# Kernel optimization log

Hardware: AMD Instinct MI355X
Metric: run time of the kernel (lower is better)

## Reference

```python
import jax, jax.numpy as jnp
import numpy as np

EPS = 1e-6      # torch F.pairwise_distance default eps (added to the difference)
MARGIN = 1.0

def _cdist_eps(a, b):
    # Exact ||a_i - b_j + eps||_2 via expansion:
    # ||a-b+eps||^2 = ||a||^2 + ||b||^2 - 2 a.b + 2*eps*(sum(a)-sum(b)) + D*eps^2
    D = a.shape[-1]
    sq = (jnp.sum(a * a, axis=1)[:, None]
          + jnp.sum(b * b, axis=1)[None, :]
          - 2.0 * (a @ b.T)
          + 2.0 * EPS * (jnp.sum(a, axis=1)[:, None] - jnp.sum(b, axis=1)[None, :])
          + D * EPS * EPS)
    return jnp.sqrt(jnp.maximum(sq, 0.0))

def setup_inputs() -> dict:
    key = jax.random.key(0)
    k1, k2, k3 = jax.random.split(key, 3)
    B, D = 4096, 1024
    return {
        'anchor_embeddings': jax.random.normal(k1, (B, D), dtype=jnp.float32),
        'positive_embeddings': jax.random.normal(k2, (B, D), dtype=jnp.float32),
        'negative_embeddings': jax.random.normal(k3, (B, D), dtype=jnp.float32),
    }

def reference(anchor_embeddings, positive_embeddings, negative_embeddings):
    a, p, n = anchor_embeddings, positive_embeddings, negative_embeddings
    # per-row anchor-positive and anchor-negative distances
    d_ap = jnp.linalg.norm(a - p + EPS, axis=-1)          # [B]
    d_an_row = jnp.linalg.norm(a - n + EPS, axis=-1)      # [B]

    # hardest negative: for each anchor, max over negatives with dist < d_ap[i], else 0
    dan_mat = _cdist_eps(a, n)                            # [B, B]
    mask_n = dan_mat < d_ap[:, None]
    hard_n = jnp.where(mask_n.any(axis=1),
                       jnp.max(jnp.where(mask_n, dan_mat, -jnp.inf), axis=1),
                       0.0)
    d_an = jnp.mean(hard_n)                               # scalar

    # hardest positive: for each anchor, min over positives with dist > d(a_i, n_i), else 0
    dpp_mat = _cdist_eps(a, p)                            # [B, B]
    mask_p = dpp_mat > d_an_row[:, None]
    hard_p = jnp.where(mask_p.any(axis=1),
                       jnp.min(jnp.where(mask_p, dpp_mat, jnp.inf), axis=1),
                       0.0)
    d_pp = jnp.mean(hard_p)                               # scalar

    loss = jnp.mean(jnp.clip(d_ap - 0.5 * d_pp - 0.5 * d_an + MARGIN, 0.0, None))
    return loss
```

## Files before the change

kernel.cpp:

```cpp
#include <hip/hip_runtime.h>


#define NB 4096
#define DIM 1024
#define EPSF 1e-6f
#define D_EPS2 (1024.0f * 1e-6f * 1e-6f)

#define BM 128
#define BK 32

typedef __bf16  bf16x8 __attribute__((ext_vector_type(8)));
typedef float   f32x4  __attribute__((ext_vector_type(4)));

__device__ __forceinline__ unsigned short f2bf(float x) {
    unsigned u = __float_as_uint(x);
    u += 0x7FFFu + ((u >> 16) & 1u);
    return (unsigned short)(u >> 16);
}

__device__ __forceinline__ void g2l16(const unsigned short* g, unsigned short* l) {
    __builtin_amdgcn_global_load_lds(
        (const __attribute__((address_space(1))) unsigned int*)g,
        (__attribute__((address_space(3))) unsigned int*)l, 16, 0, 0);
}


__global__ __launch_bounds__(256) void row_stats_kernel(
    const float* __restrict__ a, const float* __restrict__ p,
    const float* __restrict__ n,
    unsigned short* __restrict__ abf, unsigned short* __restrict__ pbf,
    unsigned short* __restrict__ nbf, float* __restrict__ stats)
{
    const int row = blockIdx.x;
    const int t   = threadIdx.x;
    const size_t base = (size_t)row * DIM;

    float4 va = ((const float4*)(a + base))[t];
    float4 vp = ((const float4*)(p + base))[t];
    float4 vn = ((const float4*)(n + base))[t];

    float v[8] = {0,0,0,0,0,0,0,0};
    const float fa[4] = {va.x, va.y, va.z, va.w};
    const float fp[4] = {vp.x, vp.y, vp.z, vp.w};
    const float fn[4] = {vn.x, vn.y, vn.z, vn.w};
#pragma unroll
    for (int e = 0; e < 4; e++) {
        v[0] += fa[e];           v[1] += fa[e] * fa[e];
        v[2] += fp[e];           v[3] += fp[e] * fp[e];
        v[4] += fn[e];           v[5] += fn[e] * fn[e];
        float dp = fa[e] - fp[e] + EPSF;  v[6] += dp * dp;
        float dn = fa[e] - fn[e] + EPSF;  v[7] += dn * dn;
    }

    ushort4 ba, bp, bn;
    ba.x = f2bf(fa[0]); ba.y = f2bf(fa[1]); ba.z = f2bf(fa[2]); ba.w = f2bf(fa[3]);
    bp.x = f2bf(fp[0]); bp.y = f2bf(fp[1]); bp.z = f2bf(fp[2]); bp.w = f2bf(fp[3]);
    bn.x = f2bf(fn[0]); bn.y = f2bf(fn[1]); bn.z = f2bf(fn[2]); bn.w = f2bf(fn[3]);
    ((ushort4*)(abf + base))[t] = ba;
    ((ushort4*)(pbf + base))[t] = bp;
    ((ushort4*)(nbf + base))[t] = bn;

#pragma unroll
    for (int m = 32; m >= 1; m >>= 1)
#pragma unroll
        for (int q = 0; q < 8; q++) v[q] += __shfl_xor(v[q], m);

    __shared__ float part[4][8];
    const int wave = t >> 6, lane = t & 63;
    if (lane == 0)
#pragma unroll
        for (int q = 0; q < 8; q++) part[wave][q] = v[q];
    __syncthreads();
    if (t == 0) {
        float r[8];
#pragma unroll
        for (int q = 0; q < 8; q++)
            r[q] = part[0][q] + part[1][q] + part[2][q] + part[3][q];
        stats[0 * NB + row] = r[1] + 2.0f * EPSF * r[0] + D_EPS2;
        stats[1 * NB + row] = r[5] - 2.0f * EPSF * r[4];
        stats[2 * NB + row] = r[3] - 2.0f * EPSF * r[2];
        stats[3 * NB + row] = sqrtf(r[6]);
        stats[4 * NB + row] = sqrtf(r[7]);
        ((unsigned*)stats)[5 * NB + row] = 0u;
        ((unsigned*)stats)[6 * NB + row] = 0x7f800000u;
    }
}

__global__ __launch_bounds__(256, 2) void gemm_mask_kernel(
    const unsigned short* __restrict__ Abf,
    const unsigned short* __restrict__ Nbf,
    const unsigned short* __restrict__ Pbf,
    float* __restrict__ stats)
{
    const int i0 = blockIdx.x * BM;
    const int j0 = blockIdx.y * BM;

    __shared__ unsigned short sA[BM * BK];
    __shared__ unsigned short sN[BM * BK];
    __shared__ unsigned short sP[BM * BK];

    const int t    = threadIdx.x;
    const int wave = t >> 6, lane = t & 63;
    const int wm   = wave >> 1, wn = wave & 1;
    const int quad = lane >> 4, lrow = lane & 15;

    const int lrow4 = lane >> 2;
    const int kch   = ((lane & 3) ^ ((lane >> 3) & 3)) * 8;
    const size_t grow = (size_t)(wave * 32 + lrow4);
    const unsigned short* ga0 = Abf + (size_t)(i0) * DIM + grow * DIM + kch;
    const unsigned short* gn0 = Nbf + (size_t)(j0) * DIM + grow * DIM + kch;
    const unsigned short* gp0 = Pbf + (size_t)(j0) * DIM + grow * DIM + kch;
    const unsigned short* ga1 = ga0 + 16 * DIM;
    const unsigned short* gn1 = gn0 + 16 * DIM;
    const unsigned short* gp1 = gp0 + 16 * DIM;
    unsigned short* la0 = sA + (wave * 32) * BK;  unsigned short* la1 = la0 + 16 * BK;
    unsigned short* ln0 = sN + (wave * 32) * BK;  unsigned short* ln1 = ln0 + 16 * BK;
    unsigned short* lp0 = sP + (wave * 32) * BK;  unsigned short* lp1 = lp0 + 16 * BK;

    const int rsw = (quad ^ ((lrow >> 1) & 3)) * 8;
    const unsigned short* pa  = sA + (wm * 64 + lrow) * BK + rsw;
    const unsigned short* pbn = sN + (wn * 64 + lrow) * BK + rsw;
    const unsigned short* pbp = sP + (wn * 64 + lrow) * BK + rsw;

    f32x4 accN[4][4], accP[4][4];
#pragma unroll
    for (int im = 0; im < 4; im++)
#pragma unroll
        for (int jn = 0; jn < 4; jn++) {
            accN[im][jn] = (f32x4)(0.0f);
            accP[im][jn] = (f32x4)(0.0f);
        }

    for (int kt = 0; kt < DIM; kt += BK) {
        __syncthreads();
        g2l16(ga0, la0);  g2l16(ga1, la1);
        g2l16(gn0, ln0);  g2l16(gn1, ln1);
        g2l16(gp0, lp0);  g2l16(gp1, lp1);
        ga0 += BK; ga1 += BK; gn0 += BK; gn1 += BK; gp0 += BK; gp1 += BK;
        __syncthreads();

        bf16x8 afr[4], bn_fr[4], bp_fr[4];
#pragma unroll
        for (int im = 0; im < 4; im++)
            afr[im] = *(const bf16x8*)(pa + im * 16 * BK);
#pragma unroll
        for (int jn = 0; jn < 4; jn++) {
            bn_fr[jn] = *(const bf16x8*)(pbn + jn * 16 * BK);
            bp_fr[jn] = *(const bf16x8*)(pbp + jn * 16 * BK);
        }
#pragma unroll
        for (int im = 0; im < 4; im++)
#pragma unroll
            for (int jn = 0; jn < 4; jn++) {
                accN[im][jn] = __builtin_amdgcn_mfma_f32_16x16x32_bf16(
                    afr[im], bn_fr[jn], accN[im][jn], 0, 0, 0);
                accP[im][jn] = __builtin_amdgcn_mfma_f32_16x16x32_bf16(
                    afr[im], bp_fr[jn], accP[im][jn], 0, 0, 0);
            }
    }

    const float* __restrict__ base_a = stats + 0 * NB;
    const float* __restrict__ cn_v   = stats + 1 * NB;
    const float* __restrict__ cp_v   = stats + 2 * NB;
    const float* __restrict__ d_ap   = stats + 3 * NB;
    const float* __restrict__ d_an   = stats + 4 * NB;
    unsigned* __restrict__ hard_n = ((unsigned*)stats) + 5 * NB;
    unsigned* __restrict__ hard_p = ((unsigned*)stats) + 6 * NB;

#pragma unroll
    for (int im = 0; im < 4; im++) {
#pragma unroll
        for (int r = 0; r < 4; r++) {
            const int gi = i0 + wm * 64 + im * 16 + quad * 4 + r;
            const float cutN = d_ap[gi];
            const float cutP = d_an[gi];
            const float bi   = base_a[gi];
            float bestN = 0.0f;
            float bestP = __uint_as_float(0x7f800000u);
#pragma unroll
            for (int jn = 0; jn < 4; jn++) {
                const int gj = j0 + wn * 64 + jn * 16 + lrow;
                const float dN = sqrtf(fmaxf(bi + cn_v[gj] - 2.0f * accN[im][jn][r], 0.0f));
                const float dP = sqrtf(fmaxf(bi + cp_v[gj] - 2.0f * accP[im][jn][r], 0.0f));
                if (dN < cutN && dN > bestN) bestN = dN;
                if (dP > cutP && dP < bestP) bestP = dP;
            }
#pragma unroll
            for (int m = 1; m < 16; m <<= 1) {
                bestN = fmaxf(bestN, __shfl_xor(bestN, m));
                bestP = fminf(bestP, __shfl_xor(bestP, m));
            }
            if (lrow == 0) {
                const unsigned bn_ = __float_as_uint(bestN);
                const unsigned bp_ = __float_as_uint(bestP);
                if (bn_ != 0u)          atomicMax(hard_n + gi, bn_);
                if (bp_ != 0x7f800000u) atomicMin(hard_p + gi, bp_);
            }
        }
    }
}

__global__ __launch_bounds__(1024) void finalize_kernel(
    const float* __restrict__ stats, float* __restrict__ out)
{
    const unsigned* hard_n = ((const unsigned*)stats) + 5 * NB;
    const unsigned* hard_p = ((const unsigned*)stats) + 6 * NB;
    const float*    d_ap   = stats + 3 * NB;
    const int t = threadIdx.x;
    const int wave = t >> 6, lane = t & 63;
    __shared__ float pn[16], pp[16];
    __shared__ float s_dan, s_dpp;

    float sn = 0.0f, sp = 0.0f;
    for (int i = t; i < NB; i += 1024) {
        sn += __uint_as_float(hard_n[i]);
        const unsigned hp = hard_p[i];
        if (hp != 0x7f800000u) sp += __uint_as_float(hp);
    }
#pragma unroll
    for (int m = 32; m >= 1; m >>= 1) {
        sn += __shfl_xor(sn, m);
        sp += __shfl_xor(sp, m);
    }
    if (lane == 0) { pn[wave] = sn; pp[wave] = sp; }
    __syncthreads();
    if (t == 0) {
        float an = 0.0f, ap = 0.0f;
#pragma unroll
        for (int w = 0; w < 16; w++) { an += pn[w]; ap += pp[w]; }
        s_dan = an / (float)NB;
        s_dpp = ap / (float)NB;
    }
    __syncthreads();
    const float dan = s_dan, dpp = s_dpp;

    float accv = 0.0f;
    for (int i = t; i < NB; i += 1024)
        accv += fmaxf(d_ap[i] - 0.5f * dpp - 0.5f * dan + 1.0f, 0.0f);
#pragma unroll
    for (int m = 32; m >= 1; m >>= 1) accv += __shfl_xor(accv, m);
    if (lane == 0) pn[wave] = accv;
    __syncthreads();
    if (t == 0) {
        float s = 0.0f;
#pragma unroll
        for (int w = 0; w < 16; w++) s += pn[w];
        out[0] = s / (float)NB;
    }
}

extern "C" void kernel_launch(void* const* d_in, const int* in_sizes, int n_in,
                              void* d_out, int out_size, void* d_ws, size_t ws_size,
                              hipStream_t stream) {
    const float* a = (const float*)d_in[0];
    const float* p = (const float*)d_in[1];
    const float* n = (const float*)d_in[2];
    float* out = (float*)d_out;

    unsigned short* abf = (unsigned short*)d_ws;
    unsigned short* pbf = abf + (size_t)NB * DIM;
    unsigned short* nbf = pbf + (size_t)NB * DIM;
    float* stats = (float*)(nbf + (size_t)NB * DIM);

    row_stats_kernel<<<NB, 256, 0, stream>>>(a, p, n, abf, pbf, nbf, stats);

    dim3 grid(NB / BM, NB / BM);
    gemm_mask_kernel<<<grid, 256, 0, stream>>>(abf, nbf, pbf, stats);

    finalize_kernel<<<1, 1024, 0, stream>>>(stats, out);
}
```

Before: 195.2 us.

## Pipeline GEMM with wave-private double-buffered LDS and register-resident A fragments

Replaces the block-shared LDS tiles and the two __syncthreads per k-step with wave-private, double-buffered LDS tiles for the N and P operands. Those tiles are loaded by global_load_lds and tracked with explicit vmcnt waits. A fragments are loaded straight from global memory into a three-stage register ring, so they skip LDS entirely. The main loop is unrolled by six so the loads for the next step overlap the MFMAs of the current one. In exchange, N and P rows are fetched twice, once by each wave row, and A reads are less coalesced. LDS use rises to 64KB per block, and the vmcnt accounting is fragile.

```diff
diff --git a/kernel.cpp b/kernel.cpp
--- a/kernel.cpp
+++ b/kernel.cpp
@@ -8,6 +8,7 @@
 
 #define BM 128
 #define BK 32
+#define NIT (DIM / BK)
 
 typedef __bf16  bf16x8 __attribute__((ext_vector_type(8)));
 typedef float   f32x4  __attribute__((ext_vector_type(4)));
@@ -23,6 +24,9 @@
         (const __attribute__((address_space(1))) unsigned int*)g,
         (__attribute__((address_space(3))) unsigned int*)l, 16, 0, 0);
 }
+
+#define WAIT_VM4  0x0F74
+#define WAIT_VM0  0x0F70
 
 
 __global__ __launch_bounds__(256) void row_stats_kernel(
@@ -95,33 +99,23 @@
     const int i0 = blockIdx.x * BM;
     const int j0 = blockIdx.y * BM;
 
-    __shared__ unsigned short sA[BM * BK];
-    __shared__ unsigned short sN[BM * BK];
-    __shared__ unsigned short sP[BM * BK];
+    __shared__ unsigned short sNP[4][2][2][64 * BK];
 
     const int t    = threadIdx.x;
     const int wave = t >> 6, lane = t & 63;
     const int wm   = wave >> 1, wn = wave & 1;
     const int quad = lane >> 4, lrow = lane & 15;
 
-    const int lrow4 = lane >> 2;
-    const int kch   = ((lane & 3) ^ ((lane >> 3) & 3)) * 8;
-    const size_t grow = (size_t)(wave * 32 + lrow4);
-    const unsigned short* ga0 = Abf + (size_t)(i0) * DIM + grow * DIM + kch;
-    const unsigned short* gn0 = Nbf + (size_t)(j0) * DIM + grow * DIM + kch;
-    const unsigned short* gp0 = Pbf + (size_t)(j0) * DIM + grow * DIM + kch;
-    const unsigned short* ga1 = ga0 + 16 * DIM;
-    const unsigned short* gn1 = gn0 + 16 * DIM;
-    const unsigned short* gp1 = gp0 + 16 * DIM;
-    unsigned short* la0 = sA + (wave * 32) * BK;  unsigned short* la1 = la0 + 16 * BK;
-    unsigned short* ln0 = sN + (wave * 32) * BK;  unsigned short* ln1 = ln0 + 16 * BK;
-    unsigned short* lp0 = sP + (wave * 32) * BK;  unsigned short* lp1 = lp0 + 16 * BK;
+    const unsigned short* gA = Abf + (size_t)(i0 + wm * 64 + lrow) * DIM + (quad << 3);
+
+    const int srow = lane >> 2;
+    const int kch  = ((lane & 3) ^ ((lane >> 3) & 3)) * 8;
+    const unsigned short* gN = Nbf + (size_t)(j0 + wn * 64 + srow) * DIM + kch;
+    const unsigned short* gP = Pbf + (size_t)(j0 + wn * 64 + srow) * DIM + kch;
 
     const int rsw = (quad ^ ((lrow >> 1) & 3)) * 8;
-    const unsigned short* pa  = sA + (wm * 64 + lrow) * BK + rsw;
-    const unsigned short* pbn = sN + (wn * 64 + lrow) * BK + rsw;
-    const unsigned short* pbp = sP + (wn * 64 + lrow) * BK + rsw;
-
+
+    bf16x8 afr[3][4];
     f32x4 accN[4][4], accP[4][4];
 #pragma unroll
     for (int im = 0; im < 4; im++)
@@ -131,33 +125,85 @@
             accP[im][jn] = (f32x4)(0.0f);
         }
 
-    for (int kt = 0; kt < DIM; kt += BK) {
-        __syncthreads();
-        g2l16(ga0, la0);  g2l16(ga1, la1);
-        g2l16(gn0, ln0);  g2l16(gn1, ln1);
-        g2l16(gp0, lp0);  g2l16(gp1, lp1);
-        ga0 += BK; ga1 += BK; gn0 += BK; gn1 += BK; gp0 += BK; gp1 += BK;
-        __syncthreads();
-
-        bf16x8 afr[4], bn_fr[4], bp_fr[4];
-#pragma unroll
-        for (int im = 0; im < 4; im++)
-            afr[im] = *(const bf16x8*)(pa + im * 16 * BK);
-#pragma unroll
-        for (int jn = 0; jn < 4; jn++) {
-            bn_fr[jn] = *(const bf16x8*)(pbn + jn * 16 * BK);
-            bp_fr[jn] = *(const bf16x8*)(pbp + jn * 16 * BK);
-        }
-#pragma unroll
-        for (int im = 0; im < 4; im++)
-#pragma unroll
-            for (int jn = 0; jn < 4; jn++) {
-                accN[im][jn] = __builtin_amdgcn_mfma_f32_16x16x32_bf16(
-                    afr[im], bn_fr[jn], accN[im][jn], 0, 0, 0);
-                accP[im][jn] = __builtin_amdgcn_mfma_f32_16x16x32_bf16(
-                    afr[im], bp_fr[jn], accP[im][jn], 0, 0, 0);
-            }
-    }
+#define ISSUE_G(k_, b_) do {                                                  \
+    const unsigned short* _gn = gN + (size_t)(k_) * BK;                       \
+    const unsigned short* _gp = gP + (size_t)(k_) * BK;                       \
+    unsigned short* _ln = &sNP[wave][(b_)][0][0];                             \
+    unsigned short* _lp = &sNP[wave][(b_)][1][0];                             \
+    g2l16(_gn,            _ln);                                               \
+    g2l16(_gn + 16 * DIM, _ln + 16 * BK);                                     \
+    g2l16(_gn + 32 * DIM, _ln + 32 * BK);                                     \
+    g2l16(_gn + 48 * DIM, _ln + 48 * BK);                                     \
+    g2l16(_gp,            _lp);                                               \
+    g2l16(_gp + 16 * DIM, _lp + 16 * BK);                                     \
+    g2l16(_gp + 32 * DIM, _lp + 32 * BK);                                     \
+    g2l16(_gp + 48 * DIM, _lp + 48 * BK);                                     \
+} while (0)
+
+#define ISSUE_A(k_, s_) do {                                                  \
+    const unsigned short* _ga = gA + (size_t)(k_) * BK;                       \
+    afr[(s_)][0] = *(const bf16x8*)(_ga);                                     \
+    afr[(s_)][1] = *(const bf16x8*)(_ga + 16 * DIM);                          \
+    afr[(s_)][2] = *(const bf16x8*)(_ga + 32 * DIM);                          \
+    afr[(s_)][3] = *(const bf16x8*)(_ga + 48 * DIM);                          \
+} while (0)
+
+#define FRAGS_MFMA(b_, s_) do {                                               \
+    bf16x8 bnfr[4], bpfr[4];                                                  \
+    _Pragma("unroll")                                                         \
+    for (int jn = 0; jn < 4; jn++) {                                          \
+        bnfr[jn] = *(const bf16x8*)(&sNP[wave][(b_)][0][(jn * 16 + lrow) * BK + rsw]); \
+        bpfr[jn] = *(const bf16x8*)(&sNP[wave][(b_)][1][(jn * 16 + lrow) * BK + rsw]); \
+    }                                                                         \
+    _Pragma("unroll")                                                         \
+    for (int im = 0; im < 4; im++)                                            \
+        _Pragma("unroll")                                                     \
+        for (int jn = 0; jn < 4; jn++) {                                      \
+            accN[im][jn] = __builtin_amdgcn_mfma_f32_16x16x32_bf16(           \
+                afr[(s_)][im], bnfr[jn], accN[im][jn], 0, 0, 0);              \
+            accP[im][jn] = __builtin_amdgcn_mfma_f32_16x16x32_bf16(           \
+                afr[(s_)][im], bpfr[jn], accP[im][jn], 0, 0, 0);              \
+        }                                                                     \
+} while (0)
+
+#define BODY(kk_) do {                                                        \
+    const int _k = k0 + (kk_);                                                \
+    __builtin_amdgcn_s_waitcnt(WAIT_VM4);                                     \
+    asm volatile("" ::: "memory");                                            \
+    ISSUE_G(_k + 1, ((kk_) + 1) & 1);                                         \
+    asm volatile("" ::: "memory");                                            \
+    ISSUE_A(_k + 2, ((kk_) + 2) % 3);                                         \
+    asm volatile("" ::: "memory");                                            \
+    FRAGS_MFMA((kk_) & 1, (kk_) % 3);                                         \
+} while (0)
+
+    ISSUE_A(0, 0);
+    asm volatile("" ::: "memory");
+    ISSUE_G(0, 0);
+    asm volatile("" ::: "memory");
+    ISSUE_A(1, 1);
+    asm volatile("" ::: "memory");
+
+    for (int k0 = 0; k0 < NIT - 2; k0 += 6) {
+        BODY(0); BODY(1); BODY(2); BODY(3); BODY(4); BODY(5);
+    }
+    {
+        __builtin_amdgcn_s_waitcnt(WAIT_VM4);
+        asm volatile("" ::: "memory");
+        ISSUE_G(NIT - 1, 1);
+        asm volatile("" ::: "memory");
+        FRAGS_MFMA(0, 0);
+    }
+    {
+        __builtin_amdgcn_s_waitcnt(WAIT_VM0);
+        asm volatile("" ::: "memory");
+        FRAGS_MFMA(1, 1);
+    }
+
+#undef BODY
+#undef FRAGS_MFMA
+#undef ISSUE_A
+#undef ISSUE_G
 
     const float* __restrict__ base_a = stats + 0 * NB;
     const float* __restrict__ cn_v   = stats + 1 * NB;
```

After: 217.9 us. 11.7% more time.
